# Optimization experiments

Hardware: AMD Instinct MI355X
Metric: run time of the kernel (lower is better)

The kernel has to match this reference:

```python
import jax, jax.numpy as jnp
import numpy as np

B, S, E = 2, 2048, 1024
H = 16
D = E // H  # head dim

def setup_inputs() -> dict:
    key = jax.random.key(0)
    ks = jax.random.split(key, 9)
    s = 1.0 / np.sqrt(E)
    return {
        "hidden_states": jax.random.normal(ks[0], (B, S, E), dtype=jnp.float32),
        "Wq": jax.random.normal(ks[1], (E, E), dtype=jnp.float32) * s,
        "bq": jnp.zeros((E,), jnp.float32),
        "Wk": jax.random.normal(ks[2], (E, E), dtype=jnp.float32) * s,
        "bk": jnp.zeros((E,), jnp.float32),
        "Wv": jax.random.normal(ks[3], (E, E), dtype=jnp.float32) * s,
        "bv": jnp.zeros((E,), jnp.float32),
        "Wo": jax.random.normal(ks[4], (E, E), dtype=jnp.float32) * s,
        "bo": jnp.zeros((E,), jnp.float32),
    }

def _split_heads(x):
    # [B,S,E] -> [B,H,S,D]
    b, s, _ = x.shape
    return x.reshape(b, s, H, D).transpose(0, 2, 1, 3)

def reference(hidden_states, Wq, bq, Wk, bk, Wv, bv, Wo, bo):
    q = _split_heads(hidden_states @ Wq + bq)  # [B,H,S,D]
    k = _split_heads(hidden_states @ Wk + bk)
    v = _split_heads(hidden_states @ Wv + bv)
    scores = jnp.einsum('bhqd,bhkd->bhqk', q, k) / jnp.sqrt(jnp.float32(D))
    probs = jax.nn.softmax(scores, axis=-1)  # [B,H,S,S]
    ctx = jnp.einsum('bhqk,bhkd->bhqd', probs, v)
    ctx = ctx.transpose(0, 2, 1, 3).reshape(hidden_states.shape[0], -1, E)
    out = ctx @ Wo + bo
    return out, probs
```

## Files before the change

kernel.cpp:

```cpp
#include <hip/hip_runtime.h>
#include <hip/hip_bf16.h>
#include <stdint.h>


typedef __attribute__((ext_vector_type(8))) short bf16x8;
typedef __attribute__((ext_vector_type(4))) short bf16x4v;
typedef __attribute__((ext_vector_type(4))) float f32x4;

#define DEV static __device__ __forceinline__

DEV short f2bs(float f) {
  union { __hip_bfloat16 b; short s; } u;
  u.b = __float2bfloat16(f);
  return u.s;
}
DEV f32x4 mfma16(bf16x8 a, bf16x8 b, f32x4 c) {
  return __builtin_amdgcn_mfma_f32_16x16x32_bf16(a, b, c, 0, 0, 0);
}
DEV float fexp2(float x) { return __builtin_amdgcn_exp2f(x); }
typedef const __attribute__((address_space(1))) void* gas1_t;
typedef __attribute__((address_space(3))) void* las3_t;
DEV void gload_lds16(const void* g, void* l) {
  __builtin_amdgcn_global_load_lds((gas1_t)(uintptr_t)g, (las3_t)(uint32_t)(uintptr_t)l,
                                   16, 0, 0);
}
#define WAIT_VMCNT(N) asm volatile("s_waitcnt vmcnt(" #N ")" ::: "memory")
#define WAIT_LGKM0() asm volatile("s_waitcnt lgkmcnt(0)" ::: "memory")
#define BARRIER() do { __builtin_amdgcn_s_barrier(); __builtin_amdgcn_sched_barrier(0); } while (0)

__global__ void cvt_all_kernel(const float* __restrict__ X,
                               const float* __restrict__ Wq, const float* __restrict__ Wk,
                               const float* __restrict__ Wv, const float* __restrict__ Wo,
                               short* __restrict__ Xb, short* __restrict__ Wt) {
  __shared__ short tile[64][68];
  int bx = blockIdx.x, t = threadIdx.x;
  if (bx < 2048) {
    size_t i = (size_t)bx * 256 + t;
    const float4* X4 = (const float4*)X;
    float4 a = X4[2 * i], c = X4[2 * i + 1];
    bf16x8 o;
    o[0] = f2bs(a.x); o[1] = f2bs(a.y); o[2] = f2bs(a.z); o[3] = f2bs(a.w);
    o[4] = f2bs(c.x); o[5] = f2bs(c.y); o[6] = f2bs(c.z); o[7] = f2bs(c.w);
    *(bf16x8*)(Xb + i * 8) = o;
    return;
  }
  int wb = bx - 2048;
  int mat = wb >> 8, rem = wb & 255;
  const float* W = mat == 0 ? Wq : mat == 1 ? Wk : mat == 2 ? Wv : Wo;
  int kb = (rem >> 4) * 64, nb = (rem & 15) * 64;
#pragma unroll
  for (int it = 0; it < 4; ++it) {
    int idx = it * 256 + t;
    int row = idx >> 4, c4 = (idx & 15) * 4;
    float4 v = *(const float4*)(W + (size_t)(kb + row) * 1024 + nb + c4);
    tile[row][c4 + 0] = f2bs(v.x); tile[row][c4 + 1] = f2bs(v.y);
    tile[row][c4 + 2] = f2bs(v.z); tile[row][c4 + 3] = f2bs(v.w);
  }
  __syncthreads();
#pragma unroll
  for (int it = 0; it < 4; ++it) {
    int idx = it * 256 + t;
    int rn = idx >> 4, c4 = (idx & 15) * 4;
    bf16x4v o;
    o[0] = tile[c4 + 0][rn]; o[1] = tile[c4 + 1][rn];
    o[2] = tile[c4 + 2][rn]; o[3] = tile[c4 + 3][rn];
    *(bf16x4v*)(Wt + (((size_t)mat) << 20) + (size_t)(nb + rn) * 1024 + kb + c4) = o;
  }
}

template <int MODE, int GBX>
__global__ __launch_bounds__(256, MODE == 0 ? 2 : 3)
void gemm_bt_kernel(const short* __restrict__ A, const short* __restrict__ Bt,
                    const float* __restrict__ bias0, const float* __restrict__ bias1,
                    const float* __restrict__ bias2,
                    short* __restrict__ o0, short* __restrict__ o1, short* __restrict__ o2,
                    float* __restrict__ fout) {
  constexpr int BN = (MODE == 0) ? 128 : 64;
  constexpr int NBLINES = BN / 32;
  __shared__ short As[2][128 * 64];
  __shared__ short Bs[2][BN * 64];
  const int nwg = GBX * gridDim.y;
  const int cpx = nwg >> 3;
  const int bid0 = blockIdx.y * GBX + blockIdx.x;
  const int bid = (bid0 % 8) * cpx + bid0 / 8;
  const int m0 = (bid % GBX) * 128, n0 = (bid / GBX) * BN;
  const int t = threadIdx.x, w = t >> 6, l = t & 63, g = l >> 4, r = l & 15;
  const int lr = l >> 3, lc = l & 7;
  const int swz = lc ^ lr;
  const int wr = (w >> 1) * 64, wc = (w & 1) * (BN / 2);
  f32x4 acc[4][BN / 32] = {};

#define STAGE_G(k0_, b_)                                                                \
  do {                                                                                  \
    _Pragma("unroll") for (int it_ = 0; it_ < 4; ++it_)                                 \
        gload_lds16(A + (size_t)(m0 + it_ * 32 + w * 8 + lr) * 1024 + (k0_) + swz * 8,  \
                    As[b_] + (it_ * 32 + w * 8) * 64);                                  \
    _Pragma("unroll") for (int it_ = 0; it_ < NBLINES; ++it_)                           \
        gload_lds16(Bt + (size_t)(n0 + it_ * 32 + w * 8 + lr) * 1024 + (k0_) + swz * 8, \
                    Bs[b_] + (it_ * 32 + w * 8) * 64);                                  \
  } while (0)

  STAGE_G(0, 0);
  for (int it = 0; it < 16; ++it) {
    const int cur = it & 1;
    if (it < 15) {
      STAGE_G((it + 1) * 64, cur ^ 1);
      if constexpr (MODE == 0) { WAIT_VMCNT(8); } else { WAIT_VMCNT(6); }
    } else {
      WAIT_VMCNT(0);
    }
    BARRIER();
    bf16x8 af[2][4], bfv[2][BN / 32];
#pragma unroll
    for (int df = 0; df < 2; df++) {
#pragma unroll
      for (int i = 0; i < 4; i++)
        af[df][i] = *(const bf16x8*)(As[cur] + (wr + i * 16 + r) * 64 +
                                     ((df * 4 + g) ^ (r & 7)) * 8);
#pragma unroll
      for (int j = 0; j < BN / 32; j++)
        bfv[df][j] = *(const bf16x8*)(Bs[cur] + (wc + j * 16 + r) * 64 +
                                      ((df * 4 + g) ^ (r & 7)) * 8);
    }
    __builtin_amdgcn_s_setprio(1);
#pragma unroll
    for (int df = 0; df < 2; df++)
#pragma unroll
      for (int i = 0; i < 4; i++)
#pragma unroll
        for (int j = 0; j < BN / 32; j++)
          acc[i][j] = mfma16(af[df][i], bfv[df][j], acc[i][j]);
    __builtin_amdgcn_s_setprio(0);
    BARRIER();
  }
#undef STAGE_G
  if constexpr (MODE == 0) {
#pragma unroll
    for (int j = 0; j < 4; j++) {
      int ng = n0 + wc + j * 16 + r;
      int mat = ng >> 10, nn = ng & 1023, hh = nn >> 6, dd = nn & 63;
      const float* bp = mat == 0 ? bias0 : (mat == 1 ? bias1 : bias2);
      short* dst = mat == 0 ? o0 : (mat == 1 ? o1 : o2);
      float bv = bp[nn];
      float sc = (mat == 0) ? 0.18033688f : 1.0f;
#pragma unroll
      for (int i = 0; i < 4; i++) {
#pragma unroll
        for (int q = 0; q < 4; q++) {
          int m = m0 + wr + i * 16 + g * 4 + q;
          int bb = m >> 11, ss = m & 2047;
          dst[((size_t)(bb * 16 + hh) * 2048 + ss) * 64 + dd] = f2bs((acc[i][j][q] + bv) * sc);
        }
      }
    }
  } else {
#pragma unroll
    for (int i = 0; i < 4; i++)
#pragma unroll
      for (int q = 0; q < 4; q++) {
        int m = m0 + wr + i * 16 + g * 4 + q;
#pragma unroll
        for (int j = 0; j < 2; j++) {
          int ng = n0 + wc + j * 16 + r;
          fout[(size_t)m * 1024 + ng] = acc[i][j][q] + bias0[ng];
        }
      }
  }
}

__global__ __launch_bounds__(256, 2)
void attn_kernel(const short* __restrict__ Qm, const short* __restrict__ Km,
                 const short* __restrict__ Vm, float* __restrict__ probs,
                 short* __restrict__ ctx) {
  __shared__ short Ks[2][128 * 64];
  __shared__ short Vt[64 * 136];
  __shared__ short Ps[4][16 * 136];
  __shared__ float rls[128];
  const int f = blockIdx.x;
  const int wgid = (f & 7) * 64 + (f >> 3);
  const int bh = wgid >> 4, q0 = (wgid & 15) * 128;
  const int bb = bh >> 4, hh = bh & 15;
  const short* Qp = Qm + (size_t)bh * 2048 * 64;
  const short* Kp = Km + (size_t)bh * 2048 * 64;
  const short* Vp = Vm + (size_t)bh * 2048 * 64;
  float* Pp = probs + (size_t)bh * 2048 * 2048;
  const int t = threadIdx.x, w = t >> 6, l = t & 63, g = l >> 4, r = l & 15;
  const int lr = l >> 3, lc = l & 7;
  const int swz = lc ^ lr;

#define STAGE_K(kt_, buf_)                                                            \
  do {                                                                                \
    const short* src_ = Kp + (size_t)((kt_) * 128) * 64;                              \
    _Pragma("unroll") for (int it_ = 0; it_ < 4; ++it_)                               \
        gload_lds16(src_ + (size_t)(it_ * 32 + w * 8 + lr) * 64 + swz * 8,            \
                    Ks[buf_] + (it_ * 32 + w * 8) * 64);                              \
  } while (0)

#pragma unroll
  for (int it = 0; it < 2; ++it) {
    gload_lds16(Qp + (size_t)(q0 + it * 32 + w * 8 + lr) * 64 + swz * 8,
                Ks[0] + (it * 32 + w * 8) * 64);
    gload_lds16(Qp + (size_t)(q0 + 64 + it * 32 + w * 8 + lr) * 64 + swz * 8,
                Ks[1] + (it * 32 + w * 8) * 64);
  }
  __syncthreads();
  bf16x8 qf0[2], qf1[2];
#pragma unroll
  for (int df = 0; df < 2; df++) {
    qf0[df] = *(const bf16x8*)(Ks[0] + (w * 16 + r) * 64 + ((df * 4 + g) ^ (r & 7)) * 8);
    qf1[df] = *(const bf16x8*)(Ks[1] + (w * 16 + r) * 64 + ((df * 4 + g) ^ (r & 7)) * 8);
  }
  WAIT_LGKM0();
  BARRIER();

  float lrow0 = 0.f, lrow1 = 0.f;
  STAGE_K(0, 0);
  for (int kt = 0; kt < 16; ++kt) {
    const int cur = kt & 1;
    if (kt < 15) {
      STAGE_K(kt + 1, cur ^ 1);
      WAIT_VMCNT(4);
    } else {
      WAIT_VMCNT(0);
    }
    BARRIER();
    f32x4 st0[8] = {}, st1[8] = {};
    __builtin_amdgcn_s_setprio(1);
#pragma unroll
    for (int df = 0; df < 2; ++df) {
      bf16x8 kf[8];
#pragma unroll
      for (int ni = 0; ni < 8; ni++)
        kf[ni] = *(const bf16x8*)(Ks[cur] + (ni * 16 + r) * 64 + ((df * 4 + g) ^ (r & 7)) * 8);
#pragma unroll
      for (int ni = 0; ni < 8; ni++) {
        st0[ni] = mfma16(kf[ni], qf0[df], st0[ni]);
        st1[ni] = mfma16(kf[ni], qf1[df], st1[ni]);
      }
    }
    __builtin_amdgcn_s_setprio(0);
    float s0 = 0.f, s1 = 0.f;
#pragma unroll
    for (int ni = 0; ni < 8; ni++)
#pragma unroll
      for (int q4 = 0; q4 < 4; q4++) {
        s0 += fexp2(st0[ni][q4]);
        s1 += fexp2(st1[ni][q4]);
      }
    s0 += __shfl_xor(s0, 16); s0 += __shfl_xor(s0, 32);
    s1 += __shfl_xor(s1, 16); s1 += __shfl_xor(s1, 32);
    lrow0 += s0;
    lrow1 += s1;
    BARRIER();
  }
  const float rinv0 = 1.0f / lrow0;
  const float rinv1 = 1.0f / lrow1;
  if (g == 0) {
    rls[w * 16 + r] = rinv0;
    rls[64 + w * 16 + r] = rinv1;
  }

  const int kp = (t >> 3) * 2, d0v = (t & 7) * 8, lcv = t & 7, kunit = t >> 5;

  f32x4 cacc0[4] = {}, cacc1[4] = {};
  STAGE_K(0, 0);
  for (int kt = 0; kt < 16; ++kt) {
    const int cur = kt & 1;
    bf16x8 v0 = *(const bf16x8*)(Vp + (size_t)(kt * 128 + kp) * 64 + d0v);
    bf16x8 v1 = *(const bf16x8*)(Vp + (size_t)(kt * 128 + kp + 1) * 64 + d0v);
    bf16x8 v2 = *(const bf16x8*)(Vp + (size_t)(kt * 128 + 64 + kp) * 64 + d0v);
    bf16x8 v3 = *(const bf16x8*)(Vp + (size_t)(kt * 128 + 64 + kp + 1) * 64 + d0v);
    if (kt < 15) STAGE_K(kt + 1, cur ^ 1);
    if (kt == 0) { WAIT_VMCNT(8); }
    else if (kt < 15) { WAIT_VMCNT(24); }
    else { WAIT_VMCNT(20); }
    BARRIER();
    f32x4 st0[8] = {}, st1[8] = {};
    __builtin_amdgcn_s_setprio(1);
#pragma unroll
    for (int df = 0; df < 2; ++df) {
      bf16x8 kf[8];
#pragma unroll
      for (int ni = 0; ni < 8; ni++)
        kf[ni] = *(const bf16x8*)(Ks[cur] + (ni * 16 + r) * 64 + ((df * 4 + g) ^ (r & 7)) * 8);
#pragma unroll
      for (int ni = 0; ni < 8; ni++) {
        st0[ni] = mfma16(kf[ni], qf0[df], st0[ni]);
        st1[ni] = mfma16(kf[ni], qf1[df], st1[ni]);
      }
    }
    __builtin_amdgcn_s_setprio(0);
    bf16x4v pk0[8], pk1[8];
#pragma unroll
    for (int ni = 0; ni < 8; ni++) {
#pragma unroll
      for (int q4 = 0; q4 < 4; q4++) {
        float p0 = fexp2(st0[ni][q4]);
        float p1 = fexp2(st1[ni][q4]);
        st0[ni][q4] = p0;
        st1[ni][q4] = p1;
        pk0[ni][q4] = f2bs(p0);
        pk1[ni][q4] = f2bs(p1);
      }
    }
#pragma unroll
    for (int e = 0; e < 8; e++) {
      unsigned int p0_ = (unsigned int)(unsigned short)v0[e] |
                         ((unsigned int)(unsigned short)v1[e] << 16);
      unsigned int p1_ = (unsigned int)(unsigned short)v2[e] |
                         ((unsigned int)(unsigned short)v3[e] << 16);
      *(unsigned int*)(Vt + (d0v + e) * 136 + ((kunit ^ lcv) << 3) + (kp & 7)) = p0_;
      *(unsigned int*)(Vt + (d0v + e) * 136 + ((8 + (kunit ^ lcv)) << 3) + (kp & 7)) = p1_;
    }
#pragma unroll
    for (int ni = 0; ni < 8; ni++)
      *(bf16x4v*)(&Ps[w][r * 136 + ni * 16 + g * 4]) = pk0[ni];
    WAIT_LGKM0();
    BARRIER();
#pragma unroll
    for (int ni = 0; ni < 8; ni++) {
      f32x4 pr;
#pragma unroll
      for (int q4 = 0; q4 < 4; q4++) pr[q4] = st0[ni][q4] * rinv0;
      *(f32x4*)(Pp + (size_t)(q0 + w * 16 + r) * 2048 + kt * 128 + ni * 16 + g * 4) = pr;
    }
    __builtin_amdgcn_s_setprio(1);
#pragma unroll
    for (int kf4 = 0; kf4 < 4; ++kf4) {
      bf16x8 pa, vb[4];
      pa = *(const bf16x8*)(&Ps[w][r * 136 + kf4 * 32 + g * 8]);
#pragma unroll
      for (int nj = 0; nj < 4; nj++) {
        int u_ = kf4 * 4 + g, x_ = nj * 2 + (r >> 3);
        int su_ = (u_ & 8) | ((u_ & 7) ^ x_);
        vb[nj] = *(const bf16x8*)(Vt + (nj * 16 + r) * 136 + (su_ << 3));
      }
#pragma unroll
      for (int nj = 0; nj < 4; nj++) cacc0[nj] = mfma16(pa, vb[nj], cacc0[nj]);
    }
    __builtin_amdgcn_s_setprio(0);
#pragma unroll
    for (int ni = 0; ni < 8; ni++)
      *(bf16x4v*)(&Ps[w][r * 136 + ni * 16 + g * 4]) = pk1[ni];
#pragma unroll
    for (int ni = 0; ni < 8; ni++) {
      f32x4 pr;
#pragma unroll
      for (int q4 = 0; q4 < 4; q4++) pr[q4] = st1[ni][q4] * rinv1;
      *(f32x4*)(Pp + (size_t)(q0 + 64 + w * 16 + r) * 2048 + kt * 128 + ni * 16 + g * 4) = pr;
    }
    __builtin_amdgcn_s_setprio(1);
#pragma unroll
    for (int kf4 = 0; kf4 < 4; ++kf4) {
      bf16x8 pa, vb[4];
      pa = *(const bf16x8*)(&Ps[w][r * 136 + kf4 * 32 + g * 8]);
#pragma unroll
      for (int nj = 0; nj < 4; nj++) {
        int u_ = kf4 * 4 + g, x_ = nj * 2 + (r >> 3);
        int su_ = (u_ & 8) | ((u_ & 7) ^ x_);
        vb[nj] = *(const bf16x8*)(Vt + (nj * 16 + r) * 136 + (su_ << 3));
      }
#pragma unroll
      for (int nj = 0; nj < 4; nj++) cacc1[nj] = mfma16(pa, vb[nj], cacc1[nj]);
    }
    __builtin_amdgcn_s_setprio(0);
  }
#pragma unroll
  for (int nj = 0; nj < 4; nj++)
#pragma unroll
    for (int q4 = 0; q4 < 4; q4++) {
      int qt = w * 16 + g * 4 + q4;
      float val0 = cacc0[nj][q4] * rls[qt];
      ctx[((size_t)(bb * 2048 + q0 + qt)) * 1024 + hh * 64 + nj * 16 + r] = f2bs(val0);
      float val1 = cacc1[nj][q4] * rls[64 + qt];
      ctx[((size_t)(bb * 2048 + q0 + 64 + qt)) * 1024 + hh * 64 + nj * 16 + r] = f2bs(val1);
    }
#undef STAGE_K
}

extern "C" void kernel_launch(void* const* d_in, const int* in_sizes, int n_in,
                              void* d_out, int out_size, void* d_ws, size_t ws_size,
                              hipStream_t stream) {
  (void)in_sizes; (void)n_in; (void)out_size; (void)ws_size;
  const float* X  = (const float*)d_in[0];
  const float* Wq = (const float*)d_in[1];
  const float* bq = (const float*)d_in[2];
  const float* Wk = (const float*)d_in[3];
  const float* bk = (const float*)d_in[4];
  const float* Wv = (const float*)d_in[5];
  const float* bv = (const float*)d_in[6];
  const float* Wo = (const float*)d_in[7];
  const float* bo = (const float*)d_in[8];
  float* out = (float*)d_out;
  float* probs = out + (size_t)2 * 2048 * 1024;

  short* Xb = (short*)d_ws;
  short* Wt = Xb + (size_t)4194304;
  short* Qb = Wt + (size_t)4194304;
  short* Kb = Qb + (size_t)4194304;
  short* Vb = Kb + (size_t)4194304;
  short* Cx = Vb + (size_t)4194304;

  cvt_all_kernel<<<3072, 256, 0, stream>>>(X, Wq, Wk, Wv, Wo, Xb, Wt);
  gemm_bt_kernel<0, 32><<<dim3(32, 24), 256, 0, stream>>>(Xb, Wt, bq, bk, bv,
                                                          Qb, Kb, Vb, nullptr);
  attn_kernel<<<512, 256, 0, stream>>>(Qb, Kb, Vb, probs, Cx);
  gemm_bt_kernel<1, 32><<<dim3(32, 16), 256, 0, stream>>>(Cx, Wt + (size_t)3 * 1048576, bo,
                                                          nullptr, nullptr, nullptr, nullptr,
                                                          nullptr, out);
}
```

Measured before the change: 222.2 us.

## Use 8 waves per attention block, one 16-row query tile per wave

The attention kernel moves from 256 to 512 threads per block, so each of 8 waves owns 16 query rows instead of 4 waves owning 32 rows each. This halves per-wave accumulators and score registers, so more waves fit per CU (launch bounds become 512,4) and K/V staging is shared by more waves. The P tile buffer shrinks and is written in two 64-column halves, while the V transpose is done once per thread for half the rows. The cost is more barrier participants and each wave reloading K fragments for fewer queries, which lowers reuse per LDS read.

```diff
diff --git a/kernel.cpp b/kernel.cpp
--- a/kernel.cpp
+++ b/kernel.cpp
@@ -168,13 +168,13 @@
   }
 }
 
-__global__ __launch_bounds__(256, 2)
+__global__ __launch_bounds__(512, 4)
 void attn_kernel(const short* __restrict__ Qm, const short* __restrict__ Km,
                  const short* __restrict__ Vm, float* __restrict__ probs,
                  short* __restrict__ ctx) {
   __shared__ short Ks[2][128 * 64];
   __shared__ short Vt[64 * 136];
-  __shared__ short Ps[4][16 * 136];
+  __shared__ short Ps[8][16 * 72];
   __shared__ float rls[128];
   const int f = blockIdx.x;
   const int wgid = (f & 7) * 64 + (f >> 3);
@@ -191,40 +191,35 @@
 #define STAGE_K(kt_, buf_)                                                            \
   do {                                                                                \
     const short* src_ = Kp + (size_t)((kt_) * 128) * 64;                              \
-    _Pragma("unroll") for (int it_ = 0; it_ < 4; ++it_)                               \
-        gload_lds16(src_ + (size_t)(it_ * 32 + w * 8 + lr) * 64 + swz * 8,            \
-                    Ks[buf_] + (it_ * 32 + w * 8) * 64);                              \
+    _Pragma("unroll") for (int it_ = 0; it_ < 2; ++it_)                               \
+        gload_lds16(src_ + (size_t)(it_ * 64 + w * 8 + lr) * 64 + swz * 8,            \
+                    Ks[buf_] + (it_ * 64 + w * 8) * 64);                              \
   } while (0)
 
 #pragma unroll
-  for (int it = 0; it < 2; ++it) {
-    gload_lds16(Qp + (size_t)(q0 + it * 32 + w * 8 + lr) * 64 + swz * 8,
-                Ks[0] + (it * 32 + w * 8) * 64);
-    gload_lds16(Qp + (size_t)(q0 + 64 + it * 32 + w * 8 + lr) * 64 + swz * 8,
-                Ks[1] + (it * 32 + w * 8) * 64);
-  }
+  for (int it = 0; it < 2; ++it)
+    gload_lds16(Qp + (size_t)(q0 + it * 64 + w * 8 + lr) * 64 + swz * 8,
+                Ks[0] + (it * 64 + w * 8) * 64);
   __syncthreads();
-  bf16x8 qf0[2], qf1[2];
-#pragma unroll
-  for (int df = 0; df < 2; df++) {
-    qf0[df] = *(const bf16x8*)(Ks[0] + (w * 16 + r) * 64 + ((df * 4 + g) ^ (r & 7)) * 8);
-    qf1[df] = *(const bf16x8*)(Ks[1] + (w * 16 + r) * 64 + ((df * 4 + g) ^ (r & 7)) * 8);
-  }
+  bf16x8 qf[2];
+#pragma unroll
+  for (int df = 0; df < 2; df++)
+    qf[df] = *(const bf16x8*)(Ks[0] + (w * 16 + r) * 64 + ((df * 4 + g) ^ (r & 7)) * 8);
   WAIT_LGKM0();
   BARRIER();
 
-  float lrow0 = 0.f, lrow1 = 0.f;
+  float lrow = 0.f;
   STAGE_K(0, 0);
   for (int kt = 0; kt < 16; ++kt) {
     const int cur = kt & 1;
     if (kt < 15) {
       STAGE_K(kt + 1, cur ^ 1);
-      WAIT_VMCNT(4);
+      WAIT_VMCNT(2);
     } else {
       WAIT_VMCNT(0);
     }
     BARRIER();
-    f32x4 st0[8] = {}, st1[8] = {};
+    f32x4 st[8] = {};
     __builtin_amdgcn_s_setprio(1);
 #pragma unroll
     for (int df = 0; df < 2; ++df) {
@@ -233,49 +228,38 @@
       for (int ni = 0; ni < 8; ni++)
         kf[ni] = *(const bf16x8*)(Ks[cur] + (ni * 16 + r) * 64 + ((df * 4 + g) ^ (r & 7)) * 8);
 #pragma unroll
-      for (int ni = 0; ni < 8; ni++) {
-        st0[ni] = mfma16(kf[ni], qf0[df], st0[ni]);
-        st1[ni] = mfma16(kf[ni], qf1[df], st1[ni]);
-      }
-    }
-    __builtin_amdgcn_s_setprio(0);
-    float s0 = 0.f, s1 = 0.f;
+      for (int ni = 0; ni < 8; ni++) st[ni] = mfma16(kf[ni], qf[df], st[ni]);
+    }
+    __builtin_amdgcn_s_setprio(0);
+    float ssum = 0.f;
 #pragma unroll
     for (int ni = 0; ni < 8; ni++)
 #pragma unroll
-      for (int q4 = 0; q4 < 4; q4++) {
-        s0 += fexp2(st0[ni][q4]);
-        s1 += fexp2(st1[ni][q4]);
-      }
-    s0 += __shfl_xor(s0, 16); s0 += __shfl_xor(s0, 32);
-    s1 += __shfl_xor(s1, 16); s1 += __shfl_xor(s1, 32);
-    lrow0 += s0;
-    lrow1 += s1;
-    BARRIER();
-  }
-  const float rinv0 = 1.0f / lrow0;
-  const float rinv1 = 1.0f / lrow1;
-  if (g == 0) {
-    rls[w * 16 + r] = rinv0;
-    rls[64 + w * 16 + r] = rinv1;
-  }
-
-  const int kp = (t >> 3) * 2, d0v = (t & 7) * 8, lcv = t & 7, kunit = t >> 5;
-
-  f32x4 cacc0[4] = {}, cacc1[4] = {};
+      for (int q4 = 0; q4 < 4; q4++) ssum += fexp2(st[ni][q4]);
+    ssum += __shfl_xor(ssum, 16);
+    ssum += __shfl_xor(ssum, 32);
+    lrow += ssum;
+    BARRIER();
+  }
+  const float rinv = 1.0f / lrow;
+  if (g == 0) rls[w * 16 + r] = rinv;
+
+  const int kp = (t >> 3) * 2;
+  const int d0v = (t & 7) * 8;
+  const int lcv = t & 7, kunit = t >> 5;
+
+  f32x4 cacc[4] = {};
   STAGE_K(0, 0);
   for (int kt = 0; kt < 16; ++kt) {
     const int cur = kt & 1;
     bf16x8 v0 = *(const bf16x8*)(Vp + (size_t)(kt * 128 + kp) * 64 + d0v);
     bf16x8 v1 = *(const bf16x8*)(Vp + (size_t)(kt * 128 + kp + 1) * 64 + d0v);
-    bf16x8 v2 = *(const bf16x8*)(Vp + (size_t)(kt * 128 + 64 + kp) * 64 + d0v);
-    bf16x8 v3 = *(const bf16x8*)(Vp + (size_t)(kt * 128 + 64 + kp + 1) * 64 + d0v);
     if (kt < 15) STAGE_K(kt + 1, cur ^ 1);
-    if (kt == 0) { WAIT_VMCNT(8); }
-    else if (kt < 15) { WAIT_VMCNT(24); }
-    else { WAIT_VMCNT(20); }
-    BARRIER();
-    f32x4 st0[8] = {}, st1[8] = {};
+    if (kt == 0) { WAIT_VMCNT(4); }
+    else if (kt < 15) { WAIT_VMCNT(12); }
+    else { WAIT_VMCNT(10); }
+    BARRIER();
+    f32x4 st[8] = {};
     __builtin_amdgcn_s_setprio(1);
 #pragma unroll
     for (int df = 0; df < 2; ++df) {
@@ -284,51 +268,60 @@
       for (int ni = 0; ni < 8; ni++)
         kf[ni] = *(const bf16x8*)(Ks[cur] + (ni * 16 + r) * 64 + ((df * 4 + g) ^ (r & 7)) * 8);
 #pragma unroll
-      for (int ni = 0; ni < 8; ni++) {
-        st0[ni] = mfma16(kf[ni], qf0[df], st0[ni]);
-        st1[ni] = mfma16(kf[ni], qf1[df], st1[ni]);
-      }
-    }
-    __builtin_amdgcn_s_setprio(0);
-    bf16x4v pk0[8], pk1[8];
+      for (int ni = 0; ni < 8; ni++) st[ni] = mfma16(kf[ni], qf[df], st[ni]);
+    }
+    __builtin_amdgcn_s_setprio(0);
+    bf16x4v pk[8];
 #pragma unroll
     for (int ni = 0; ni < 8; ni++) {
 #pragma unroll
       for (int q4 = 0; q4 < 4; q4++) {
-        float p0 = fexp2(st0[ni][q4]);
-        float p1 = fexp2(st1[ni][q4]);
-        st0[ni][q4] = p0;
-        st1[ni][q4] = p1;
-        pk0[ni][q4] = f2bs(p0);
-        pk1[ni][q4] = f2bs(p1);
-      }
-    }
+        float pe = fexp2(st[ni][q4]);
+        st[ni][q4] = pe;
+        pk[ni][q4] = f2bs(pe);
+      }
+    }
+#pragma unroll
+    for (int ni = 0; ni < 4; ni++)
+      *(bf16x4v*)(&Ps[w][r * 72 + ni * 16 + g * 4]) = pk[ni];
 #pragma unroll
     for (int e = 0; e < 8; e++) {
-      unsigned int p0_ = (unsigned int)(unsigned short)v0[e] |
+      unsigned int pv_ = (unsigned int)(unsigned short)v0[e] |
                          ((unsigned int)(unsigned short)v1[e] << 16);
-      unsigned int p1_ = (unsigned int)(unsigned short)v2[e] |
-                         ((unsigned int)(unsigned short)v3[e] << 16);
-      *(unsigned int*)(Vt + (d0v + e) * 136 + ((kunit ^ lcv) << 3) + (kp & 7)) = p0_;
-      *(unsigned int*)(Vt + (d0v + e) * 136 + ((8 + (kunit ^ lcv)) << 3) + (kp & 7)) = p1_;
-    }
-#pragma unroll
-    for (int ni = 0; ni < 8; ni++)
-      *(bf16x4v*)(&Ps[w][r * 136 + ni * 16 + g * 4]) = pk0[ni];
+      int su_ = (kunit & 8) | ((kunit & 7) ^ lcv);
+      *(unsigned int*)(Vt + (d0v + e) * 136 + (su_ << 3) + (kp & 7)) = pv_;
+    }
     WAIT_LGKM0();
     BARRIER();
 #pragma unroll
     for (int ni = 0; ni < 8; ni++) {
       f32x4 pr;
 #pragma unroll
-      for (int q4 = 0; q4 < 4; q4++) pr[q4] = st0[ni][q4] * rinv0;
+      for (int q4 = 0; q4 < 4; q4++) pr[q4] = st[ni][q4] * rinv;
       *(f32x4*)(Pp + (size_t)(q0 + w * 16 + r) * 2048 + kt * 128 + ni * 16 + g * 4) = pr;
     }
     __builtin_amdgcn_s_setprio(1);
 #pragma unroll
-    for (int kf4 = 0; kf4 < 4; ++kf4) {
+    for (int kf4 = 0; kf4 < 2; ++kf4) {
       bf16x8 pa, vb[4];
-      pa = *(const bf16x8*)(&Ps[w][r * 136 + kf4 * 32 + g * 8]);
+      pa = *(const bf16x8*)(&Ps[w][r * 72 + kf4 * 32 + g * 8]);
+#pragma unroll
+      for (int nj = 0; nj < 4; nj++) {
+        int u_ = kf4 * 4 + g, x_ = nj * 2 + (r >> 3);
+        vb[nj] = *(const bf16x8*)(Vt + (nj * 16 + r) * 136 + ((u_ ^ x_) << 3));
+      }
+#pragma unroll
+      for (int nj = 0; nj < 4; nj++) cacc[nj] = mfma16(pa, vb[nj], cacc[nj]);
+    }
+    __builtin_amdgcn_s_setprio(0);
+#pragma unroll
+    for (int ni = 4; ni < 8; ni++)
+      *(bf16x4v*)(&Ps[w][r * 72 + (ni - 4) * 16 + g * 4]) = pk[ni];
+    __builtin_amdgcn_s_setprio(1);
+#pragma unroll
+    for (int kf4 = 2; kf4 < 4; ++kf4) {
+      bf16x8 pa, vb[4];
+      pa = *(const bf16x8*)(&Ps[w][r * 72 + (kf4 - 2) * 32 + g * 8]);
 #pragma unroll
       for (int nj = 0; nj < 4; nj++) {
         int u_ = kf4 * 4 + g, x_ = nj * 2 + (r >> 3);
@@ -336,32 +329,7 @@
         vb[nj] = *(const bf16x8*)(Vt + (nj * 16 + r) * 136 + (su_ << 3));
       }
 #pragma unroll
-      for (int nj = 0; nj < 4; nj++) cacc0[nj] = mfma16(pa, vb[nj], cacc0[nj]);
-    }
-    __builtin_amdgcn_s_setprio(0);
-#pragma unroll
-    for (int ni = 0; ni < 8; ni++)
-      *(bf16x4v*)(&Ps[w][r * 136 + ni * 16 + g * 4]) = pk1[ni];
-#pragma unroll
-    for (int ni = 0; ni < 8; ni++) {
-      f32x4 pr;
-#pragma unroll
-      for (int q4 = 0; q4 < 4; q4++) pr[q4] = st1[ni][q4] * rinv1;
-      *(f32x4*)(Pp + (size_t)(q0 + 64 + w * 16 + r) * 2048 + kt * 128 + ni * 16 + g * 4) = pr;
-    }
-    __builtin_amdgcn_s_setprio(1);
-#pragma unroll
-    for (int kf4 = 0; kf4 < 4; ++kf4) {
-      bf16x8 pa, vb[4];
-      pa = *(const bf16x8*)(&Ps[w][r * 136 + kf4 * 32 + g * 8]);
-#pragma unroll
-      for (int nj = 0; nj < 4; nj++) {
-        int u_ = kf4 * 4 + g, x_ = nj * 2 + (r >> 3);
-        int su_ = (u_ & 8) | ((u_ & 7) ^ x_);
-        vb[nj] = *(const bf16x8*)(Vt + (nj * 16 + r) * 136 + (su_ << 3));
-      }
-#pragma unroll
-      for (int nj = 0; nj < 4; nj++) cacc1[nj] = mfma16(pa, vb[nj], cacc1[nj]);
+      for (int nj = 0; nj < 4; nj++) cacc[nj] = mfma16(pa, vb[nj], cacc[nj]);
     }
     __builtin_amdgcn_s_setprio(0);
   }
@@ -370,10 +338,8 @@
 #pragma unroll
     for (int q4 = 0; q4 < 4; q4++) {
       int qt = w * 16 + g * 4 + q4;
-      float val0 = cacc0[nj][q4] * rls[qt];
-      ctx[((size_t)(bb * 2048 + q0 + qt)) * 1024 + hh * 64 + nj * 16 + r] = f2bs(val0);
-      float val1 = cacc1[nj][q4] * rls[64 + qt];
-      ctx[((size_t)(bb * 2048 + q0 + 64 + qt)) * 1024 + hh * 64 + nj * 16 + r] = f2bs(val1);
+      float val = cacc[nj][q4] * rls[qt];
+      ctx[((size_t)(bb * 2048 + q0 + qt)) * 1024 + hh * 64 + nj * 16 + r] = f2bs(val);
     }
 #undef STAGE_K
 }
@@ -404,7 +370,7 @@
   cvt_all_kernel<<<3072, 256, 0, stream>>>(X, Wq, Wk, Wv, Wo, Xb, Wt);
   gemm_bt_kernel<0, 32><<<dim3(32, 24), 256, 0, stream>>>(Xb, Wt, bq, bk, bv,
                                                           Qb, Kb, Vb, nullptr);
-  attn_kernel<<<512, 256, 0, stream>>>(Qb, Kb, Vb, probs, Cx);
+  attn_kernel<<<512, 512, 0, stream>>>(Qb, Kb, Vb, probs, Cx);
   gemm_bt_kernel<1, 32><<<dim3(32, 16), 256, 0, stream>>>(Cx, Wt + (size_t)3 * 1048576, bo,
                                                           nullptr, nullptr, nullptr, nullptr,
                                                           nullptr, out);
```

After: 234.6 us. 5.6% more time.
